# Kernel optimization log

Hardware: AMD Instinct MI355X
Metric: run time of the kernel (lower is better)

Reference implementation:

```python
import jax, jax.numpy as jnp
import numpy as np

K, B, S, D, V, H = 4, 64, 50, 256, 40000, 4
DH = D // H
TOPK = 2
NEG = -1e9
SCALE = float(1.0 / np.sqrt(DH))


def setup_inputs() -> dict:
    key = jax.random.key(0)
    ks = jax.random.split(key, 16)
    s = 0.05
    return {
        "ids":   jax.random.randint(ks[0], (K, B, S), 0, V),
        "items": jax.random.randint(ks[1], (K, B, S), 0, V),
        "adj":   jax.random.randint(ks[2], (B, S, S), 0, 5),
        "alias": jax.random.randint(ks[3], (B, S), 0, S),
        "eps":   jax.random.normal(ks[4], (B, S, K), jnp.float32),
        "emb":   jax.random.normal(ks[5], (K, V, D), jnp.float32) * s,
        "agg_a": jax.random.normal(ks[6], (K, 4, D), jnp.float32) * s,
        "Wq": jax.random.normal(ks[7], (K, D, D), jnp.float32) * s,
        "Wk": jax.random.normal(ks[8], (K, D, D), jnp.float32) * s,
        "Wv": jax.random.normal(ks[9], (K, D, D), jnp.float32) * s,
        "Wo": jax.random.normal(ks[10], (K, D, D), jnp.float32) * s,
        "ln1_g": jnp.ones((K, D), jnp.float32),
        "ln1_b": jnp.zeros((K, D), jnp.float32),
        "W1": jax.random.normal(ks[11], (K, D, 4 * D), jnp.float32) * s,
        "W2": jax.random.normal(ks[12], (K, 4 * D, D), jnp.float32) * s,
        "ln2_g": jnp.ones((K, D), jnp.float32),
        "ln2_b": jnp.zeros((K, D), jnp.float32),
        "Wg": jax.random.normal(ks[13], (D, K), jnp.float32) * s,
        "Wn": jax.random.normal(ks[14], (D, K), jnp.float32) * s,
    }


def _layer_norm(x, g, b):
    m = jnp.mean(x, -1, keepdims=True)
    v = jnp.var(x, -1, keepdims=True)
    return (x - m) * jax.lax.rsqrt(v + 1e-5) * g + b


def _per_key(ids, items, emb, a, Wq, Wk, Wv, Wo, g1, b1, W1, W2, g2, b2, adj, alias):
    hg = emb[items]                                          # [B,S,D] graph-node embeddings
    # LocalAggregator: relation-typed pairwise attention over session graph (adj in {1..4})
    e = jnp.einsum('bid,bjd,rd->rbij', hg, hg, a)            # [4,B,S,S], avoids [B,S,S,D]
    e = jax.nn.leaky_relu(e, 0.2)
    alpha = jnp.full(adj.shape, NEG, e.dtype)
    for r in range(4):
        alpha = jnp.where(adj == r + 1, e[r], alpha)
    alpha = jax.nn.softmax(alpha, -1)
    h_local = jnp.einsum('bij,bjd->bid', alpha, hg)          # graph aggregation
    h = jnp.take_along_axis(h_local, alias[..., None], axis=1)   # distribute graph rows to sequence
    # memory-transformer block (pre-LN causal MHA + FFN)
    x = _layer_norm(h, g1, b1)
    q = (x @ Wq).reshape(B, S, H, DH)
    k = (x @ Wk).reshape(B, S, H, DH)
    v = (x @ Wv).reshape(B, S, H, DH)
    scores = jnp.einsum('bihd,bjhd->bhij', q, k) * SCALE
    causal = jnp.tril(jnp.ones((S, S), bool))
    scores = jnp.where(causal, scores, NEG)
    attn = jax.nn.softmax(scores, -1)
    o = jnp.einsum('bhij,bjhd->bihd', attn, v).reshape(B, S, D) @ Wo
    h = h + o
    y = _layer_norm(h, g2, b2)
    h = h + jax.nn.gelu(y @ W1) @ W2
    return h


def reference(ids, items, adj, alias, eps, emb, agg_a, Wq, Wk, Wv, Wo,
              ln1_g, ln1_b, W1, W2, ln2_g, ln2_b, Wg, Wn):
    per_key = jax.vmap(_per_key, in_axes=(0,) * 14 + (None, None))
    h_keys = per_key(ids, items, emb, agg_a, Wq, Wk, Wv, Wo,
                     ln1_g, ln1_b, W1, W2, ln2_g, ln2_b, adj, alias)   # [K,B,S,D]
    # gate input: mean over per-key input-sequence embeddings (h_seq in original)
    h_seq = jax.vmap(lambda e, i: e[i])(emb, ids).mean(0)              # [B,S,D]
    # noisy top-k gating over node-type experts
    logits = h_seq @ Wg + jax.nn.softplus(h_seq @ Wn) * eps            # [B,S,K]
    top_v, top_i = jax.lax.top_k(logits, TOPK)
    w = jax.nn.softmax(top_v, -1)                                      # [B,S,TOPK]
    gates = jnp.sum(jax.nn.one_hot(top_i, K, dtype=w.dtype) * w[..., None], axis=-2)  # [B,S,K]
    return jnp.einsum('bsk,kbsd->bsd', gates, h_keys)
```

## Files before the change

kernel.cpp:

```cpp
#include <hip/hip_runtime.h>
#include <hip/hip_bf16.h>
#include <math.h>

#define K_ 4
#define B_ 64
#define S_ 50
#define D_ 256
#define V_ 40000
#define H_ 4
#define DH_ 64
#define NEG_ (-1e9f)
#define SCALE_ 0.125f

typedef __attribute__((ext_vector_type(8))) __bf16 bf16x8v;
typedef __attribute__((ext_vector_type(4))) float f32x4v;

__device__ __forceinline__ float wred_sum(float v) {
#pragma unroll
  for (int off = 32; off > 0; off >>= 1) v += __shfl_xor(v, off, 64);
  return v;
}
__device__ __forceinline__ float wred_max(float v) {
#pragma unroll
  for (int off = 32; off > 0; off >>= 1) v = fmaxf(v, __shfl_xor(v, off, 64));
  return v;
}
__device__ __forceinline__ float softplusf(float x) {
  return (x > 20.f) ? x : log1pf(expf(x));
}
__device__ __forceinline__ float geluf(float x) {
  const float c = 0.7978845608028654f;
  float x3 = x * x * x;
  return 0.5f * x * (1.f + tanhf(c * (x + 0.044715f * x3)));
}
__device__ __forceinline__ float bf2f(unsigned int u) {
  return __uint_as_float(u << 16);
}
__device__ __forceinline__ unsigned short f2bf(float f) {
  unsigned u = __float_as_uint(f);
  return (unsigned short)((u + 0x7fffu + ((u >> 16) & 1u)) >> 16);
}
__device__ __forceinline__ bf16x8v cvt8(float4 a, float4 b) {
  bf16x8v r;
  r[0] = (__bf16)a.x; r[1] = (__bf16)a.y; r[2] = (__bf16)a.z; r[3] = (__bf16)a.w;
  r[4] = (__bf16)b.x; r[5] = (__bf16)b.y; r[6] = (__bf16)b.z; r[7] = (__bf16)b.w;
  return r;
}

__global__ __launch_bounds__(256) void front_kernel(
    const int* __restrict__ items, const int* __restrict__ adj,
    const float* __restrict__ emb, const float* __restrict__ agg_a,
    const int* __restrict__ alias_, float* __restrict__ hbuf,
    unsigned short* __restrict__ xb,
    const float* __restrict__ ln1g, const float* __restrict__ ln1b,
    const int* __restrict__ ids, const float* __restrict__ Wg,
    const float* __restrict__ Wn, const float* __restrict__ eps,
    float* __restrict__ gates,
    const float* __restrict__ wq, const float* __restrict__ wk,
    const float* __restrict__ wv, const float* __restrict__ wo,
    const float* __restrict__ w1, const float* __restrict__ w2,
    unsigned short* __restrict__ wqkvT, unsigned short* __restrict__ woT,
    unsigned short* __restrict__ w1T, unsigned short* __restrict__ w2T) {
  __shared__ __align__(16) char smem[62816];
  int bid = blockIdx.x;
  int t = threadIdx.x;

  if (bid < 256) {
    typedef __bf16 (*arr264)[264];
    arr264 hgb = (arr264)smem;
    float (*e_f)[68] = (float(*)[68])(smem + 33792);
    unsigned char (*adj_s)[64] = (unsigned char(*)[64])(smem + 47392);
    arr264 a_sb = (arr264)(smem + 51488);
    __bf16 (*alp)[72] = (__bf16(*)[72])(smem + 53600);
    float* hl = (float*)smem;

    int kb = bid;
    int k = kb >> 6, b = kb & 63;
    for (int c = t; c < 2048; c += 256) {
      int row = c >> 5, c8 = (c & 31) * 8;
      bf16x8v val;
      if (row < S_) {
        int g = items[kb * S_ + row];
        const float* src = emb + ((long)k * V_ + g) * D_ + c8;
        val = cvt8(*(const float4*)src, *(const float4*)(src + 4));
      } else {
#pragma unroll
        for (int e = 0; e < 8; ++e) val[e] = (__bf16)0.f;
      }
      *(bf16x8v*)&hgb[row][c8] = val;
    }
    if (t < 128) {
      int row = t >> 5, c8 = (t & 31) * 8;
      const float* src = agg_a + ((long)k * 4 + row) * D_ + c8;
      *(bf16x8v*)&a_sb[row][c8] = cvt8(*(const float4*)src, *(const float4*)(src + 4));
    }
    for (int c = t; c < 4096; c += 256) {
      int i = c >> 6, j = c & 63;
      adj_s[i][j] = (i < S_ && j < S_)
                        ? (unsigned char)adj[((long)b * S_ + i) * S_ + j] : 0;
    }
    __syncthreads();
    int w = t >> 6, lane = t & 63;
    int m16 = lane & 15, quad = lane >> 4;
    float e_sel[4][4];
#pragma unroll
    for (int nt = 0; nt < 4; ++nt)
#pragma unroll
      for (int rg = 0; rg < 4; ++rg) e_sel[nt][rg] = NEG_;
#pragma unroll
    for (int r = 0; r < 4; ++r) {
      f32x4v acc[4];
#pragma unroll
      for (int nt = 0; nt < 4; ++nt) acc[nt] = (f32x4v){0.f, 0.f, 0.f, 0.f};
#pragma unroll
      for (int k0 = 0; k0 < 8; ++k0) {
        int kc = k0 * 32 + quad * 8;
        bf16x8v hr = *(const bf16x8v*)&hgb[w * 16 + m16][kc];
        bf16x8v ar = *(const bf16x8v*)&a_sb[r][kc];
        bf16x8v af;
#pragma unroll
        for (int e = 0; e < 8; ++e) af[e] = (__bf16)((float)hr[e] * (float)ar[e]);
#pragma unroll
        for (int nt = 0; nt < 4; ++nt) {
          bf16x8v bf = *(const bf16x8v*)&hgb[nt * 16 + m16][kc];
          acc[nt] = __builtin_amdgcn_mfma_f32_16x16x32_bf16(af, bf, acc[nt], 0, 0, 0);
        }
      }
#pragma unroll
      for (int nt = 0; nt < 4; ++nt)
#pragma unroll
        for (int rg = 0; rg < 4; ++rg) {
          int i = w * 16 + quad * 4 + rg, j = nt * 16 + m16;
          if (adj_s[i][j] == r + 1) {
            float v = acc[nt][rg];
            e_sel[nt][rg] = (v >= 0.f) ? v : 0.2f * v;
          }
        }
    }
#pragma unroll
    for (int nt = 0; nt < 4; ++nt)
#pragma unroll
      for (int rg = 0; rg < 4; ++rg) {
        int i = w * 16 + quad * 4 + rg;
        if (i < S_) e_f[i][nt * 16 + m16] = e_sel[nt][rg];
      }
    __syncthreads();
    for (int i = w; i < S_; i += 4) {
      float val = (lane < S_) ? e_f[i][lane] : -INFINITY;
      float m = wred_max(val);
      float p = expf(val - m);
      float ssum = wred_sum(p);
      alp[i][lane] = (__bf16)(p / ssum);
    }
    __syncthreads();
    f32x4v acc16[16];
#pragma unroll
    for (int nt = 0; nt < 16; ++nt) {
      f32x4v acc = (f32x4v){0.f, 0.f, 0.f, 0.f};
#pragma unroll
      for (int k0 = 0; k0 < 2; ++k0) {
        int jb = k0 * 32 + quad * 8;
        bf16x8v af = *(const bf16x8v*)&alp[w * 16 + m16][jb];
        bf16x8v bf;
#pragma unroll
        for (int tt = 0; tt < 8; ++tt) bf[tt] = hgb[jb + tt][nt * 16 + m16];
        acc = __builtin_amdgcn_mfma_f32_16x16x32_bf16(af, bf, acc, 0, 0, 0);
      }
      acc16[nt] = acc;
    }
    __syncthreads();
#pragma unroll
    for (int nt = 0; nt < 16; ++nt)
#pragma unroll
      for (int rg = 0; rg < 4; ++rg) {
        int i = w * 16 + quad * 4 + rg;
        if (i < S_) hl[i * 260 + nt * 16 + m16] = acc16[nt][rg];
      }
    __syncthreads();
    for (int s = w; s < S_; s += 4) {
      int src = alias_[b * S_ + s];
      const float4 v = *(const float4*)&hl[src * 260 + lane * 4];
      long off = ((long)kb * S_ + s) * D_ + lane * 4;
      *(float4*)(hbuf + off) = v;
      float sum = wred_sum(v.x + v.y + v.z + v.w);
      float sq = wred_sum(v.x * v.x + v.y * v.y + v.z * v.z + v.w * v.w);
      float mean = sum * (1.f / D_);
      float var = sq * (1.f / D_) - mean * mean;
      float rs = rsqrtf(var + 1e-5f);
      const float4 gv = *(const float4*)(ln1g + k * D_ + lane * 4);
      const float4 bv = *(const float4*)(ln1b + k * D_ + lane * 4);
      ushort4 o;
      o.x = f2bf((v.x - mean) * rs * gv.x + bv.x);
      o.y = f2bf((v.y - mean) * rs * gv.y + bv.y);
      o.z = f2bf((v.z - mean) * rs * gv.z + bv.z);
      o.w = f2bf((v.w - mean) * rs * gv.w + bv.w);
      *(ushort4*)(xb + off) = o;
    }
    return;
  }

  if (bid < 1024) {
    int tid = bid - 256;
    typedef unsigned short row66[66];
    row66* tile = (row66*)smem;
    const float* src; unsigned short* dst; int C, R; int r0, c0;
    if (tid < 192) {
      int sect = tid >> 6; int rem = tid & 63;
      int k = rem >> 4, t2 = rem & 15;
      r0 = (t2 >> 2) * 64; c0 = (t2 & 3) * 64;
      src = ((sect == 0) ? wq : (sect == 1) ? wk : wv) + (long)k * 65536;
      dst = wqkvT + ((long)k * 768 + sect * 256) * 256;
      R = 256; C = 256;
    } else if (tid < 256) {
      int rem = tid - 192; int k = rem >> 4, t2 = rem & 15;
      r0 = (t2 >> 2) * 64; c0 = (t2 & 3) * 64;
      src = wo + (long)k * 65536; dst = woT + (long)k * 65536;
      R = 256; C = 256;
    } else if (tid < 512) {
      int rem = tid - 256; int k = rem >> 6, t2 = rem & 63;
      r0 = (t2 >> 4) * 64; c0 = (t2 & 15) * 64;
      src = w1 + (long)k * 262144; dst = w1T + (long)k * 262144;
      R = 256; C = 1024;
    } else {
      int rem = tid - 512; int k = rem >> 6, t2 = rem & 63;
      r0 = (t2 >> 2) * 64; c0 = (t2 & 3) * 64;
      src = w2 + (long)k * 262144; dst = w2T + (long)k * 262144;
      R = 1024; C = 256;
    }
    int sr = t >> 2, sc = (t & 3) * 16;
    const float* p = src + (long)(r0 + sr) * C + c0 + sc;
#pragma unroll
    for (int q = 0; q < 4; ++q) {
      float4 f = *(const float4*)(p + q * 4);
      tile[sr][sc + q * 4 + 0] = f2bf(f.x);
      tile[sr][sc + q * 4 + 1] = f2bf(f.y);
      tile[sr][sc + q * 4 + 2] = f2bf(f.z);
      tile[sr][sc + q * 4 + 3] = f2bf(f.w);
    }
    __syncthreads();
    int dc = t >> 2, ch = (t & 3) * 16;
    unsigned int wds[8];
#pragma unroll
    for (int i = 0; i < 8; ++i)
      wds[i] = (unsigned int)tile[ch + 2 * i][dc] |
               ((unsigned int)tile[ch + 2 * i + 1][dc] << 16);
    unsigned short* dp = dst + (long)(c0 + dc) * R + r0 + ch;
    uint4 o0 = make_uint4(wds[0], wds[1], wds[2], wds[3]);
    uint4 o1 = make_uint4(wds[4], wds[5], wds[6], wds[7]);
    *(uint4*)dp = o0;
    *(uint4*)(dp + 8) = o1;
    return;
  }

  {
    int w = t >> 6, lane = t & 63;
    int item = (bid - 1024) * 4 + w;
    int b = item / S_, s = item % S_;
    int d0 = lane * 4;
    float4 hs = make_float4(0.f, 0.f, 0.f, 0.f);
#pragma unroll
    for (int k = 0; k < K_; ++k) {
      int id = ids[(k * B_ + b) * S_ + s];
      const float4 e = *(const float4*)(emb + ((long)k * V_ + id) * D_ + d0);
      hs.x += e.x; hs.y += e.y; hs.z += e.z; hs.w += e.w;
    }
    hs.x *= 0.25f; hs.y *= 0.25f; hs.z *= 0.25f; hs.w *= 0.25f;
    float logit[4];
#pragma unroll
    for (int j = 0; j < K_; ++j) {
      float pg = hs.x * Wg[(d0 + 0) * K_ + j] + hs.y * Wg[(d0 + 1) * K_ + j] +
                 hs.z * Wg[(d0 + 2) * K_ + j] + hs.w * Wg[(d0 + 3) * K_ + j];
      float pn = hs.x * Wn[(d0 + 0) * K_ + j] + hs.y * Wn[(d0 + 1) * K_ + j] +
                 hs.z * Wn[(d0 + 2) * K_ + j] + hs.w * Wn[(d0 + 3) * K_ + j];
      pg = wred_sum(pg);
      pn = wred_sum(pn);
      logit[j] = pg + softplusf(pn) * eps[item * K_ + j];
    }
    if (lane == 0) {
      int i0 = 0; float v0 = logit[0];
      for (int j = 1; j < K_; ++j) if (logit[j] > v0) { v0 = logit[j]; i0 = j; }
      int i1 = -1; float v1 = 0.f;
      for (int j = 0; j < K_; ++j)
        if (j != i0 && (i1 < 0 || logit[j] > v1)) { v1 = logit[j]; i1 = j; }
      float w0 = 1.f / (1.f + expf(v1 - v0));
      float w1 = 1.f - w0;
#pragma unroll
      for (int j = 0; j < K_; ++j)
        gates[item * K_ + j] = (j == i0) ? w0 : ((j == i1) ? w1 : 0.f);
    }
  }
}

__global__ __launch_bounds__(256) void bgemm3(
    const unsigned short* __restrict__ A, const unsigned short* __restrict__ Bt,
    long strideA, long strideBt, int N, int Kd,
    unsigned short* __restrict__ Cb, long strideCb, int act) {
  __shared__ unsigned short sA[128][72];
  __shared__ unsigned short sB[128][72];
  int z = blockIdx.z;
  A += (long)z * strideA;
  Bt += (long)z * strideBt;
  int t = threadIdx.x, w = t >> 6, lane = t & 63;
  int wr = w >> 1, wc = w & 1;
  int row0 = blockIdx.y * 128, col0 = blockIdx.x * 128;
  int m16 = lane & 15, quad = lane >> 4;
  f32x4v acc[4][4];
#pragma unroll
  for (int mr = 0; mr < 4; ++mr)
#pragma unroll
    for (int nr = 0; nr < 4; ++nr) acc[mr][nr] = (f32x4v){0.f, 0.f, 0.f, 0.f};
  int sr = t >> 1, sc = (t & 1) * 32;
  const unsigned short* pa = A + (long)(row0 + sr) * Kd + sc;
  const unsigned short* pb = Bt + (long)(col0 + sr) * Kd + sc;
  uint4 a0 = *(const uint4*)(pa);
  uint4 a1 = *(const uint4*)(pa + 8);
  uint4 a2 = *(const uint4*)(pa + 16);
  uint4 a3 = *(const uint4*)(pa + 24);
  uint4 b0 = *(const uint4*)(pb);
  uint4 b1 = *(const uint4*)(pb + 8);
  uint4 b2 = *(const uint4*)(pb + 16);
  uint4 b3 = *(const uint4*)(pb + 24);
  for (int k0 = 0; k0 < Kd; k0 += 64) {
    __syncthreads();
    *(uint4*)&sA[sr][sc] = a0;
    *(uint4*)&sA[sr][sc + 8] = a1;
    *(uint4*)&sA[sr][sc + 16] = a2;
    *(uint4*)&sA[sr][sc + 24] = a3;
    *(uint4*)&sB[sr][sc] = b0;
    *(uint4*)&sB[sr][sc + 8] = b1;
    *(uint4*)&sB[sr][sc + 16] = b2;
    *(uint4*)&sB[sr][sc + 24] = b3;
    if (k0 + 64 < Kd) {
      a0 = *(const uint4*)(pa + k0 + 64);
      a1 = *(const uint4*)(pa + k0 + 72);
      a2 = *(const uint4*)(pa + k0 + 80);
      a3 = *(const uint4*)(pa + k0 + 88);
      b0 = *(const uint4*)(pb + k0 + 64);
      b1 = *(const uint4*)(pb + k0 + 72);
      b2 = *(const uint4*)(pb + k0 + 80);
      b3 = *(const uint4*)(pb + k0 + 88);
    }
    __syncthreads();
#pragma unroll
    for (int half = 0; half < 2; ++half) {
      int kg = half * 32 + quad * 8;
      bf16x8v af[4], bf[4];
#pragma unroll
      for (int i = 0; i < 4; ++i) {
        af[i] = *(const bf16x8v*)&sA[wr * 64 + i * 16 + m16][kg];
        bf[i] = *(const bf16x8v*)&sB[wc * 64 + i * 16 + m16][kg];
      }
#pragma unroll
      for (int mr = 0; mr < 4; ++mr)
#pragma unroll
        for (int nr = 0; nr < 4; ++nr)
          acc[mr][nr] = __builtin_amdgcn_mfma_f32_16x16x32_bf16(
              af[mr], bf[nr], acc[mr][nr], 0, 0, 0);
    }
  }
#pragma unroll
  for (int mr = 0; mr < 4; ++mr) {
    int rbase = row0 + wr * 64 + mr * 16 + quad * 4;
#pragma unroll
    for (int nr = 0; nr < 4; ++nr) {
      int col = col0 + wc * 64 + nr * 16 + m16;
#pragma unroll
      for (int i2 = 0; i2 < 4; ++i2) {
        float vv = acc[mr][nr][i2];
        if (act == 1) vv = geluf(vv);
        Cb[(long)z * strideCb + (long)(rbase + i2) * N + col] = f2bf(vv);
      }
    }
  }
}

__global__ __launch_bounds__(256) void attn_mfma(
    const unsigned short* __restrict__ qkv, unsigned short* __restrict__ o) {
  __shared__ __bf16 qs[64][72], ks[64][72], vs[64][72];
  __shared__ __bf16 psh[64][72], psl[64][72];
  int idx = blockIdx.x;
  int h = idx & 3;
  int kb = idx >> 2;
  long base = (long)kb * S_ * 768 + h * DH_;
  int t = threadIdx.x;
  for (int f = t; f < 512; f += 256) {
    int row = f >> 3, c8 = (f & 7) * 8;
    uint4 zq = make_uint4(0, 0, 0, 0), zk = zq, zv = zq;
    if (row < S_) {
      long g = base + (long)row * 768 + c8;
      zq = *(const uint4*)(qkv + g);
      zk = *(const uint4*)(qkv + g + 256);
      zv = *(const uint4*)(qkv + g + 512);
    }
    *(uint4*)&qs[row][c8] = zq;
    *(uint4*)&ks[row][c8] = zk;
    *(uint4*)&vs[row][c8] = zv;
  }
  __syncthreads();
  int w = t >> 6, lane = t & 63;
  int m16 = lane & 15, quad = lane >> 4;
  f32x4v sacc[4];
#pragma unroll
  for (int nt = 0; nt < 4; ++nt) sacc[nt] = (f32x4v){0.f, 0.f, 0.f, 0.f};
#pragma unroll
  for (int k0 = 0; k0 < 2; ++k0) {
    int kc = k0 * 32 + quad * 8;
    bf16x8v af = *(const bf16x8v*)&qs[w * 16 + m16][kc];
#pragma unroll
    for (int nt = 0; nt < 4; ++nt) {
      bf16x8v bf = *(const bf16x8v*)&ks[nt * 16 + m16][kc];
      sacc[nt] = __builtin_amdgcn_mfma_f32_16x16x32_bf16(af, bf, sacc[nt], 0, 0, 0);
    }
  }
#pragma unroll
  for (int rg = 0; rg < 4; ++rg) {
    int i = w * 16 + quad * 4 + rg;
    float v4[4];
    if (i < S_) {
      float mx = -INFINITY;
#pragma unroll
      for (int nt = 0; nt < 4; ++nt) {
        int j = nt * 16 + m16;
        float vv = (j <= i) ? sacc[nt][rg] * SCALE_ : -INFINITY;
        v4[nt] = vv;
        mx = fmaxf(mx, vv);
      }
#pragma unroll
      for (int off = 1; off < 16; off <<= 1)
        mx = fmaxf(mx, __shfl_xor(mx, off, 64));
      float sum = 0.f;
#pragma unroll
      for (int nt = 0; nt < 4; ++nt) {
        v4[nt] = expf(v4[nt] - mx);
        sum += v4[nt];
      }
#pragma unroll
      for (int off = 1; off < 16; off <<= 1) sum += __shfl_xor(sum, off, 64);
      float inv = 1.f / sum;
#pragma unroll
      for (int nt = 0; nt < 4; ++nt) v4[nt] *= inv;
    } else {
#pragma unroll
      for (int nt = 0; nt < 4; ++nt) v4[nt] = 0.f;
    }
#pragma unroll
    for (int nt = 0; nt < 4; ++nt) {
      __bf16 hi = (__bf16)v4[nt];
      psh[i][nt * 16 + m16] = hi;
      psl[i][nt * 16 + m16] = (__bf16)(v4[nt] - (float)hi);
    }
  }
  __syncthreads();
  f32x4v oacc[4];
#pragma unroll
  for (int nt = 0; nt < 4; ++nt) oacc[nt] = (f32x4v){0.f, 0.f, 0.f, 0.f};
#pragma unroll
  for (int k0 = 0; k0 < 2; ++k0) {
    int jb = k0 * 32 + quad * 8;
    bf16x8v ah = *(const bf16x8v*)&psh[w * 16 + m16][jb];
    bf16x8v al = *(const bf16x8v*)&psl[w * 16 + m16][jb];
#pragma unroll
    for (int nt = 0; nt < 4; ++nt) {
      bf16x8v bf;
#pragma unroll
      for (int tt = 0; tt < 8; ++tt) bf[tt] = vs[jb + tt][nt * 16 + m16];
      oacc[nt] = __builtin_amdgcn_mfma_f32_16x16x32_bf16(ah, bf, oacc[nt], 0, 0, 0);
      oacc[nt] = __builtin_amdgcn_mfma_f32_16x16x32_bf16(al, bf, oacc[nt], 0, 0, 0);
    }
  }
#pragma unroll
  for (int nt = 0; nt < 4; ++nt)
#pragma unroll
    for (int rg = 0; rg < 4; ++rg) {
      int i = w * 16 + quad * 4 + rg;
      if (i < S_)
        o[((long)kb * S_ + i) * D_ + h * DH_ + nt * 16 + m16] = f2bf(oacc[nt][rg]);
    }
}

__global__ __launch_bounds__(256) void bgemm_oln(
    const unsigned short* __restrict__ A, const unsigned short* __restrict__ Bt,
    float* __restrict__ hbuf, unsigned short* __restrict__ y,
    const float* __restrict__ g2, const float* __restrict__ b2) {
  __shared__ unsigned short sA[64][72];
  __shared__ unsigned short sB[256][72];
  const long BSD = (long)B_ * S_ * D_;
  int z = blockIdx.z;
  const unsigned short* Ap = A + (long)z * BSD;
  const unsigned short* Bp = Bt + (long)z * 65536;
  int t = threadIdx.x, w = t >> 6, lane = t & 63;
  int row0 = blockIdx.x * 64;
  int m16 = lane & 15, quad = lane >> 4;
  f32x4v acc[16];
#pragma unroll
  for (int nt = 0; nt < 16; ++nt) acc[nt] = (f32x4v){0.f, 0.f, 0.f, 0.f};
  int sr = t >> 2, sc = (t & 3) * 16;
  const unsigned short* pa = Ap + (long)(row0 + sr) * 256 + sc;
  const unsigned short* pb = Bp + (long)sr * 256 + sc;
  uint4 a0 = *(const uint4*)pa;
  uint4 a1 = *(const uint4*)(pa + 8);
  uint4 bv[8];
#pragma unroll
  for (int q = 0; q < 4; ++q) {
    bv[2 * q] = *(const uint4*)(pb + q * 16384);
    bv[2 * q + 1] = *(const uint4*)(pb + q * 16384 + 8);
  }
  for (int k0 = 0; k0 < 256; k0 += 64) {
    __syncthreads();
    *(uint4*)&sA[sr][sc] = a0;
    *(uint4*)&sA[sr][sc + 8] = a1;
#pragma unroll
    for (int q = 0; q < 4; ++q) {
      *(uint4*)&sB[q * 64 + sr][sc] = bv[2 * q];
      *(uint4*)&sB[q * 64 + sr][sc + 8] = bv[2 * q + 1];
    }
    if (k0 + 64 < 256) {
      a0 = *(const uint4*)(pa + k0 + 64);
      a1 = *(const uint4*)(pa + k0 + 72);
#pragma unroll
      for (int q = 0; q < 4; ++q) {
        bv[2 * q] = *(const uint4*)(pb + q * 16384 + k0 + 64);
        bv[2 * q + 1] = *(const uint4*)(pb + q * 16384 + k0 + 72);
      }
    }
    __syncthreads();
#pragma unroll
    for (int half = 0; half < 2; ++half) {
      int kg = half * 32 + quad * 8;
      bf16x8v af = *(const bf16x8v*)&sA[w * 16 + m16][kg];
#pragma unroll
      for (int nt = 0; nt < 16; ++nt) {
        bf16x8v bf = *(const bf16x8v*)&sB[nt * 16 + m16][kg];
        acc[nt] = __builtin_amdgcn_mfma_f32_16x16x32_bf16(af, bf, acc[nt], 0, 0, 0);
      }
    }
  }
  long zoff = (long)z * BSD;
  int rbase = row0 + w * 16 + quad * 4;
#pragma unroll
  for (int nt = 0; nt < 16; ++nt)
#pragma unroll
    for (int i2 = 0; i2 < 4; ++i2) {
      long off = zoff + (long)(rbase + i2) * 256 + nt * 16 + m16;
      float vv = acc[nt][i2] + hbuf[off];
      acc[nt][i2] = vv;
      hbuf[off] = vv;
    }
  float mean[4], rstd[4];
#pragma unroll
  for (int i2 = 0; i2 < 4; ++i2) {
    float s = 0.f, q = 0.f;
#pragma unroll
    for (int nt = 0; nt < 16; ++nt) {
      float vv = acc[nt][i2];
      s += vv; q += vv * vv;
    }
#pragma unroll
    for (int off = 1; off < 16; off <<= 1) {
      s += __shfl_xor(s, off, 64);
      q += __shfl_xor(q, off, 64);
    }
    float m = s * (1.f / D_);
    float var = q * (1.f / D_) - m * m;
    mean[i2] = m;
    rstd[i2] = rsqrtf(var + 1e-5f);
  }
#pragma unroll
  for (int nt = 0; nt < 16; ++nt) {
    float gv = g2[z * D_ + nt * 16 + m16];
    float bvv = b2[z * D_ + nt * 16 + m16];
#pragma unroll
    for (int i2 = 0; i2 < 4; ++i2) {
      long off = zoff + (long)(rbase + i2) * 256 + nt * 16 + m16;
      y[off] = f2bf((acc[nt][i2] - mean[i2]) * rstd[i2] * gv + bvv);
    }
  }
}

__global__ __launch_bounds__(256) void bgemm_f2a(
    const unsigned short* __restrict__ A, const unsigned short* __restrict__ Bt,
    const float* __restrict__ hbuf, const float* __restrict__ gates,
    float* __restrict__ out) {
  __shared__ unsigned short sA[64][72];
  __shared__ unsigned short sB[64][72];
  const long T4 = 3276800;
  const long BSD = (long)B_ * S_ * D_;
  int z = blockIdx.z;
  int t = threadIdx.x, w = t >> 6, lane = t & 63;
  int col0 = blockIdx.x * 64, row0 = blockIdx.y * 64;
  int m16 = lane & 15, quad = lane >> 4;
  f32x4v acc[4];
#pragma unroll
  for (int nt = 0; nt < 4; ++nt) acc[nt] = (f32x4v){0.f, 0.f, 0.f, 0.f};
  int sr = t >> 2, sc = (t & 3) * 16;
  const unsigned short* pa = A + (long)z * T4 + (long)(row0 + sr) * 1024 + sc;
  const unsigned short* pb = Bt + (long)z * 262144 + (long)(col0 + sr) * 1024 + sc;
  uint4 a0 = *(const uint4*)pa;
  uint4 a1 = *(const uint4*)(pa + 8);
  uint4 b0 = *(const uint4*)pb;
  uint4 b1 = *(const uint4*)(pb + 8);
  for (int k0 = 0; k0 < 1024; k0 += 64) {
    __syncthreads();
    *(uint4*)&sA[sr][sc] = a0;
    *(uint4*)&sA[sr][sc + 8] = a1;
    *(uint4*)&sB[sr][sc] = b0;
    *(uint4*)&sB[sr][sc + 8] = b1;
    if (k0 + 64 < 1024) {
      a0 = *(const uint4*)(pa + k0 + 64);
      a1 = *(const uint4*)(pa + k0 + 72);
      b0 = *(const uint4*)(pb + k0 + 64);
      b1 = *(const uint4*)(pb + k0 + 72);
    }
    __syncthreads();
#pragma unroll
    for (int half = 0; half < 2; ++half) {
      int kg = half * 32 + quad * 8;
      bf16x8v af = *(const bf16x8v*)&sA[w * 16 + m16][kg];
#pragma unroll
      for (int nt = 0; nt < 4; ++nt) {
        bf16x8v bf = *(const bf16x8v*)&sB[nt * 16 + m16][kg];
        acc[nt] = __builtin_amdgcn_mfma_f32_16x16x32_bf16(af, bf, acc[nt], 0, 0, 0);
      }
    }
  }
  int rbase = row0 + w * 16 + quad * 4;
#pragma unroll
  for (int i2 = 0; i2 < 4; ++i2) {
    float gz = gates[(rbase + i2) * 4 + z];
    if (gz != 0.f) {
#pragma unroll
      for (int nt = 0; nt < 4; ++nt) {
        long off = (long)(rbase + i2) * 256 + col0 + nt * 16 + m16;
        float vv = gz * (acc[nt][i2] + hbuf[(long)z * BSD + off]);
        atomicAdd(&out[off], vv);
      }
    }
  }
}

extern "C" void kernel_launch(void* const* d_in, const int* in_sizes, int n_in,
                              void* d_out, int out_size, void* d_ws,
                              size_t ws_size, hipStream_t stream) {
  const int* ids = (const int*)d_in[0];
  const int* items = (const int*)d_in[1];
  const int* adj = (const int*)d_in[2];
  const int* alias = (const int*)d_in[3];
  const float* eps = (const float*)d_in[4];
  const float* emb = (const float*)d_in[5];
  const float* agg_a = (const float*)d_in[6];
  const float* Wq = (const float*)d_in[7];
  const float* Wk = (const float*)d_in[8];
  const float* Wv = (const float*)d_in[9];
  const float* Wo = (const float*)d_in[10];
  const float* ln1g = (const float*)d_in[11];
  const float* ln1b = (const float*)d_in[12];
  const float* W1 = (const float*)d_in[13];
  const float* W2 = (const float*)d_in[14];
  const float* ln2g = (const float*)d_in[15];
  const float* ln2b = (const float*)d_in[16];
  const float* Wg = (const float*)d_in[17];
  const float* Wn = (const float*)d_in[18];
  float* out = (float*)d_out;

  const long BSD = (long)B_ * S_ * D_;
  float* ws = (float*)d_ws;
  float* gates = ws;
  float* hbuf = ws + 16384;
  unsigned short* ub = (unsigned short*)(ws + 16384 + 4 * BSD);
  unsigned short* xb = ub;
  unsigned short* qkvb = ub + 3276800;
  unsigned short* tb = qkvb;
  unsigned short* wqkvT = ub + 16384000;
  unsigned short* woT = wqkvT + 786432;
  unsigned short* w1T = woT + 262144;
  unsigned short* w2T = w1T + 1048576;

  const long T4 = 3276800;

  hipMemsetAsync(out, 0, (size_t)BSD * sizeof(float), stream);

  front_kernel<<<1824, 256, 0, stream>>>(
      items, adj, emb, agg_a, alias, hbuf, xb, ln1g, ln1b,
      ids, Wg, Wn, eps, gates,
      Wq, Wk, Wv, Wo, W1, W2, wqkvT, woT, w1T, w2T);
  bgemm3<<<dim3(6, 25, 4), 256, 0, stream>>>(xb, wqkvT, BSD, 196608, 768, 256,
      qkvb, 2457600, 0);
  attn_mfma<<<K_ * B_ * H_, 256, 0, stream>>>(qkvb, xb);
  bgemm_oln<<<dim3(50, 1, 4), 256, 0, stream>>>(xb, woT, hbuf, xb, ln2g, ln2b);
  bgemm3<<<dim3(8, 25, 4), 256, 0, stream>>>(xb, w1T, BSD, 262144, 1024, 256,
      tb, T4, 1);
  bgemm_f2a<<<dim3(4, 50, 4), 256, 0, stream>>>(tb, w2T, hbuf, gates, out);
}
```

Baseline: 398.0 us.

## Fuse QKV projection into attention and fuse the whole post-attention tail per (key,batch)

The QKV GEMM is folded into the attention kernel: each (key,batch,head) block computes its Q, K and V tiles straight into LDS from bf16 activations and weights read from global memory. The output projection, residual add, LayerNorm, FFN1 with GELU, FFN2 and the gated atomic accumulation are merged into a single kernel with one block per (key,batch), so the hidden activation stays in LDS. This removes three launches and the global round trips for qkv, o, y and the 1024-wide FFN intermediate. In exchange the tail runs only 256 blocks with weights streamed from global/L2 without LDS staging, which risks low occupancy and latency-bound GEMMs. Activation reads for rows 50 to 63 of each tile run past the valid sequence rows.

```diff
diff --git a/kernel.cpp b/kernel.cpp
--- a/kernel.cpp
+++ b/kernel.cpp
@@ -32,9 +32,6 @@
   const float c = 0.7978845608028654f;
   float x3 = x * x * x;
   return 0.5f * x * (1.f + tanhf(c * (x + 0.044715f * x3)));
-}
-__device__ __forceinline__ float bf2f(unsigned int u) {
-  return __uint_as_float(u << 16);
 }
 __device__ __forceinline__ unsigned short f2bf(float f) {
   unsigned u = __float_as_uint(f);
@@ -291,114 +288,45 @@
   }
 }
 
-__global__ __launch_bounds__(256) void bgemm3(
-    const unsigned short* __restrict__ A, const unsigned short* __restrict__ Bt,
-    long strideA, long strideBt, int N, int Kd,
-    unsigned short* __restrict__ Cb, long strideCb, int act) {
-  __shared__ unsigned short sA[128][72];
-  __shared__ unsigned short sB[128][72];
-  int z = blockIdx.z;
-  A += (long)z * strideA;
-  Bt += (long)z * strideBt;
-  int t = threadIdx.x, w = t >> 6, lane = t & 63;
-  int wr = w >> 1, wc = w & 1;
-  int row0 = blockIdx.y * 128, col0 = blockIdx.x * 128;
-  int m16 = lane & 15, quad = lane >> 4;
-  f32x4v acc[4][4];
-#pragma unroll
-  for (int mr = 0; mr < 4; ++mr)
-#pragma unroll
-    for (int nr = 0; nr < 4; ++nr) acc[mr][nr] = (f32x4v){0.f, 0.f, 0.f, 0.f};
-  int sr = t >> 1, sc = (t & 1) * 32;
-  const unsigned short* pa = A + (long)(row0 + sr) * Kd + sc;
-  const unsigned short* pb = Bt + (long)(col0 + sr) * Kd + sc;
-  uint4 a0 = *(const uint4*)(pa);
-  uint4 a1 = *(const uint4*)(pa + 8);
-  uint4 a2 = *(const uint4*)(pa + 16);
-  uint4 a3 = *(const uint4*)(pa + 24);
-  uint4 b0 = *(const uint4*)(pb);
-  uint4 b1 = *(const uint4*)(pb + 8);
-  uint4 b2 = *(const uint4*)(pb + 16);
-  uint4 b3 = *(const uint4*)(pb + 24);
-  for (int k0 = 0; k0 < Kd; k0 += 64) {
-    __syncthreads();
-    *(uint4*)&sA[sr][sc] = a0;
-    *(uint4*)&sA[sr][sc + 8] = a1;
-    *(uint4*)&sA[sr][sc + 16] = a2;
-    *(uint4*)&sA[sr][sc + 24] = a3;
-    *(uint4*)&sB[sr][sc] = b0;
-    *(uint4*)&sB[sr][sc + 8] = b1;
-    *(uint4*)&sB[sr][sc + 16] = b2;
-    *(uint4*)&sB[sr][sc + 24] = b3;
-    if (k0 + 64 < Kd) {
-      a0 = *(const uint4*)(pa + k0 + 64);
-      a1 = *(const uint4*)(pa + k0 + 72);
-      a2 = *(const uint4*)(pa + k0 + 80);
-      a3 = *(const uint4*)(pa + k0 + 88);
-      b0 = *(const uint4*)(pb + k0 + 64);
-      b1 = *(const uint4*)(pb + k0 + 72);
-      b2 = *(const uint4*)(pb + k0 + 80);
-      b3 = *(const uint4*)(pb + k0 + 88);
-    }
-    __syncthreads();
-#pragma unroll
-    for (int half = 0; half < 2; ++half) {
-      int kg = half * 32 + quad * 8;
-      bf16x8v af[4], bf[4];
-#pragma unroll
-      for (int i = 0; i < 4; ++i) {
-        af[i] = *(const bf16x8v*)&sA[wr * 64 + i * 16 + m16][kg];
-        bf[i] = *(const bf16x8v*)&sB[wc * 64 + i * 16 + m16][kg];
-      }
-#pragma unroll
-      for (int mr = 0; mr < 4; ++mr)
-#pragma unroll
-        for (int nr = 0; nr < 4; ++nr)
-          acc[mr][nr] = __builtin_amdgcn_mfma_f32_16x16x32_bf16(
-              af[mr], bf[nr], acc[mr][nr], 0, 0, 0);
-    }
-  }
-#pragma unroll
-  for (int mr = 0; mr < 4; ++mr) {
-    int rbase = row0 + wr * 64 + mr * 16 + quad * 4;
-#pragma unroll
-    for (int nr = 0; nr < 4; ++nr) {
-      int col = col0 + wc * 64 + nr * 16 + m16;
-#pragma unroll
-      for (int i2 = 0; i2 < 4; ++i2) {
-        float vv = acc[mr][nr][i2];
-        if (act == 1) vv = geluf(vv);
-        Cb[(long)z * strideCb + (long)(rbase + i2) * N + col] = f2bf(vv);
-      }
-    }
-  }
-}
-
-__global__ __launch_bounds__(256) void attn_mfma(
-    const unsigned short* __restrict__ qkv, unsigned short* __restrict__ o) {
+__global__ __launch_bounds__(256) void qkv_attn(
+    const unsigned short* __restrict__ xb,
+    const unsigned short* __restrict__ wqkvT,
+    unsigned short* __restrict__ ob) {
   __shared__ __bf16 qs[64][72], ks[64][72], vs[64][72];
   __shared__ __bf16 psh[64][72], psl[64][72];
   int idx = blockIdx.x;
-  int h = idx & 3;
-  int kb = idx >> 2;
-  long base = (long)kb * S_ * 768 + h * DH_;
-  int t = threadIdx.x;
-  for (int f = t; f < 512; f += 256) {
-    int row = f >> 3, c8 = (f & 7) * 8;
-    uint4 zq = make_uint4(0, 0, 0, 0), zk = zq, zv = zq;
-    if (row < S_) {
-      long g = base + (long)row * 768 + c8;
-      zq = *(const uint4*)(qkv + g);
-      zk = *(const uint4*)(qkv + g + 256);
-      zv = *(const uint4*)(qkv + g + 512);
-    }
-    *(uint4*)&qs[row][c8] = zq;
-    *(uint4*)&ks[row][c8] = zk;
-    *(uint4*)&vs[row][c8] = zv;
+  int h = idx & 3, kb = idx >> 2;
+  int k = kb >> 6;
+  int t = threadIdx.x, w = t >> 6, lane = t & 63;
+  int m16 = lane & 15, quad = lane >> 4;
+  const unsigned short* xrow = xb + (long)kb * S_ * D_;
+#pragma unroll
+  for (int sect = 0; sect < 3; ++sect) {
+    f32x4v acc[4];
+#pragma unroll
+    for (int mr = 0; mr < 4; ++mr) acc[mr] = (f32x4v){0.f, 0.f, 0.f, 0.f};
+    const unsigned short* wrow =
+        wqkvT + ((long)k * 768 + sect * 256 + h * 64 + w * 16 + m16) * 256;
+#pragma unroll
+    for (int st = 0; st < 8; ++st) {
+      int kc = st * 32 + quad * 8;
+      bf16x8v bf = *(const bf16x8v*)(wrow + kc);
+#pragma unroll
+      for (int mr = 0; mr < 4; ++mr) {
+        bf16x8v af = *(const bf16x8v*)(xrow + (long)(mr * 16 + m16) * 256 + kc);
+        acc[mr] = __builtin_amdgcn_mfma_f32_16x16x32_bf16(af, bf, acc[mr], 0, 0, 0);
+      }
+    }
+    __bf16 (*dst)[72] = (sect == 0) ? qs : (sect == 1) ? ks : vs;
+#pragma unroll
+    for (int mr = 0; mr < 4; ++mr)
+#pragma unroll
+      for (int i2 = 0; i2 < 4; ++i2)
+        dst[mr * 16 + quad * 4 + i2][w * 16 + m16] = (__bf16)acc[mr][i2];
   }
   __syncthreads();
-  int w = t >> 6, lane = t & 63;
-  int m16 = lane & 15, quad = lane >> 4;
+  for (int c = t; c < 14 * 72; c += 256) vs[50 + c / 72][c % 72] = (__bf16)0.f;
+  __syncthreads();
   f32x4v sacc[4];
 #pragma unroll
   for (int nt = 0; nt < 4; ++nt) sacc[nt] = (f32x4v){0.f, 0.f, 0.f, 0.f};
@@ -474,168 +402,165 @@
     for (int rg = 0; rg < 4; ++rg) {
       int i = w * 16 + quad * 4 + rg;
       if (i < S_)
-        o[((long)kb * S_ + i) * D_ + h * DH_ + nt * 16 + m16] = f2bf(oacc[nt][rg]);
-    }
-}
-
-__global__ __launch_bounds__(256) void bgemm_oln(
-    const unsigned short* __restrict__ A, const unsigned short* __restrict__ Bt,
-    float* __restrict__ hbuf, unsigned short* __restrict__ y,
-    const float* __restrict__ g2, const float* __restrict__ b2) {
-  __shared__ unsigned short sA[64][72];
-  __shared__ unsigned short sB[256][72];
-  const long BSD = (long)B_ * S_ * D_;
-  int z = blockIdx.z;
-  const unsigned short* Ap = A + (long)z * BSD;
-  const unsigned short* Bp = Bt + (long)z * 65536;
+        ob[((long)kb * S_ + i) * D_ + h * DH_ + nt * 16 + m16] = f2bf(oacc[nt][rg]);
+    }
+}
+
+__global__ __launch_bounds__(256) void tail_fused(
+    const unsigned short* __restrict__ ob, const unsigned short* __restrict__ woT,
+    const unsigned short* __restrict__ w1T, const unsigned short* __restrict__ w2T,
+    const float* __restrict__ hbuf, const float* __restrict__ gates,
+    const float* __restrict__ g2, const float* __restrict__ b2,
+    float* __restrict__ out) {
+  __shared__ __bf16 ybuf[64][264];
+  __shared__ __bf16 ts[64][136];
+  __shared__ float lnS[4][64], lnQ[4][64];
+  int kb = blockIdx.x;
+  int k = kb >> 6, b = kb & 63;
   int t = threadIdx.x, w = t >> 6, lane = t & 63;
-  int row0 = blockIdx.x * 64;
   int m16 = lane & 15, quad = lane >> 4;
-  f32x4v acc[16];
-#pragma unroll
-  for (int nt = 0; nt < 16; ++nt) acc[nt] = (f32x4v){0.f, 0.f, 0.f, 0.f};
-  int sr = t >> 2, sc = (t & 3) * 16;
-  const unsigned short* pa = Ap + (long)(row0 + sr) * 256 + sc;
-  const unsigned short* pb = Bp + (long)sr * 256 + sc;
-  uint4 a0 = *(const uint4*)pa;
-  uint4 a1 = *(const uint4*)(pa + 8);
-  uint4 bv[8];
-#pragma unroll
-  for (int q = 0; q < 4; ++q) {
-    bv[2 * q] = *(const uint4*)(pb + q * 16384);
-    bv[2 * q + 1] = *(const uint4*)(pb + q * 16384 + 8);
-  }
-  for (int k0 = 0; k0 < 256; k0 += 64) {
-    __syncthreads();
-    *(uint4*)&sA[sr][sc] = a0;
-    *(uint4*)&sA[sr][sc + 8] = a1;
-#pragma unroll
-    for (int q = 0; q < 4; ++q) {
-      *(uint4*)&sB[q * 64 + sr][sc] = bv[2 * q];
-      *(uint4*)&sB[q * 64 + sr][sc + 8] = bv[2 * q + 1];
-    }
-    if (k0 + 64 < 256) {
-      a0 = *(const uint4*)(pa + k0 + 64);
-      a1 = *(const uint4*)(pa + k0 + 72);
-#pragma unroll
-      for (int q = 0; q < 4; ++q) {
-        bv[2 * q] = *(const uint4*)(pb + q * 16384 + k0 + 64);
-        bv[2 * q + 1] = *(const uint4*)(pb + q * 16384 + k0 + 72);
-      }
-    }
-    __syncthreads();
-#pragma unroll
-    for (int half = 0; half < 2; ++half) {
-      int kg = half * 32 + quad * 8;
-      bf16x8v af = *(const bf16x8v*)&sA[w * 16 + m16][kg];
-#pragma unroll
-      for (int nt = 0; nt < 16; ++nt) {
-        bf16x8v bf = *(const bf16x8v*)&sB[nt * 16 + m16][kg];
-        acc[nt] = __builtin_amdgcn_mfma_f32_16x16x32_bf16(af, bf, acc[nt], 0, 0, 0);
-      }
-    }
-  }
-  long zoff = (long)z * BSD;
-  int rbase = row0 + w * 16 + quad * 4;
-#pragma unroll
-  for (int nt = 0; nt < 16; ++nt)
+  for (int c = t; c < 14 * 264; c += 256) ybuf[50 + c / 264][c % 264] = (__bf16)0.f;
+  f32x4v v[4][4];
+#pragma unroll
+  for (int mr = 0; mr < 4; ++mr)
+#pragma unroll
+    for (int nt = 0; nt < 4; ++nt) v[mr][nt] = (f32x4v){0.f, 0.f, 0.f, 0.f};
+  const unsigned short* orow = ob + (long)kb * S_ * D_;
+#pragma unroll
+  for (int st = 0; st < 8; ++st) {
+    int kc = st * 32 + quad * 8;
+    bf16x8v bfv[4];
+#pragma unroll
+    for (int nt = 0; nt < 4; ++nt)
+      bfv[nt] = *(const bf16x8v*)(woT + ((long)k * 256 + w * 64 + nt * 16 + m16) * 256 + kc);
+#pragma unroll
+    for (int mr = 0; mr < 4; ++mr) {
+      bf16x8v af = *(const bf16x8v*)(orow + (long)(mr * 16 + m16) * 256 + kc);
+#pragma unroll
+      for (int nt = 0; nt < 4; ++nt)
+        v[mr][nt] = __builtin_amdgcn_mfma_f32_16x16x32_bf16(af, bfv[nt], v[mr][nt], 0, 0, 0);
+    }
+  }
+  long hb = (long)kb * S_ * D_;
+#pragma unroll
+  for (int mr = 0; mr < 4; ++mr)
 #pragma unroll
     for (int i2 = 0; i2 < 4; ++i2) {
-      long off = zoff + (long)(rbase + i2) * 256 + nt * 16 + m16;
-      float vv = acc[nt][i2] + hbuf[off];
-      acc[nt][i2] = vv;
-      hbuf[off] = vv;
-    }
-  float mean[4], rstd[4];
-#pragma unroll
-  for (int i2 = 0; i2 < 4; ++i2) {
-    float s = 0.f, q = 0.f;
-#pragma unroll
-    for (int nt = 0; nt < 16; ++nt) {
-      float vv = acc[nt][i2];
-      s += vv; q += vv * vv;
-    }
-#pragma unroll
-    for (int off = 1; off < 16; off <<= 1) {
-      s += __shfl_xor(s, off, 64);
-      q += __shfl_xor(q, off, 64);
-    }
-    float m = s * (1.f / D_);
-    float var = q * (1.f / D_) - m * m;
-    mean[i2] = m;
-    rstd[i2] = rsqrtf(var + 1e-5f);
-  }
-#pragma unroll
-  for (int nt = 0; nt < 16; ++nt) {
-    float gv = g2[z * D_ + nt * 16 + m16];
-    float bvv = b2[z * D_ + nt * 16 + m16];
+      int row = mr * 16 + quad * 4 + i2;
+      float s = 0.f, q = 0.f;
+#pragma unroll
+      for (int nt = 0; nt < 4; ++nt) {
+        int col = w * 64 + nt * 16 + m16;
+        float hv = (row < S_) ? hbuf[hb + (long)row * 256 + col] : 0.f;
+        float vv = v[mr][nt][i2] + hv;
+        v[mr][nt][i2] = vv;
+        s += vv; q += vv * vv;
+      }
+#pragma unroll
+      for (int off = 1; off < 16; off <<= 1) {
+        s += __shfl_xor(s, off, 64);
+        q += __shfl_xor(q, off, 64);
+      }
+      if (m16 == 0) { lnS[w][row] = s; lnQ[w][row] = q; }
+    }
+  __syncthreads();
+  float gv[4], bvv[4];
+#pragma unroll
+  for (int nt = 0; nt < 4; ++nt) {
+    int col = w * 64 + nt * 16 + m16;
+    gv[nt] = g2[k * D_ + col];
+    bvv[nt] = b2[k * D_ + col];
+  }
+#pragma unroll
+  for (int mr = 0; mr < 4; ++mr)
 #pragma unroll
     for (int i2 = 0; i2 < 4; ++i2) {
-      long off = zoff + (long)(rbase + i2) * 256 + nt * 16 + m16;
-      y[off] = f2bf((acc[nt][i2] - mean[i2]) * rstd[i2] * gv + bvv);
-    }
-  }
-}
-
-__global__ __launch_bounds__(256) void bgemm_f2a(
-    const unsigned short* __restrict__ A, const unsigned short* __restrict__ Bt,
-    const float* __restrict__ hbuf, const float* __restrict__ gates,
-    float* __restrict__ out) {
-  __shared__ unsigned short sA[64][72];
-  __shared__ unsigned short sB[64][72];
-  const long T4 = 3276800;
-  const long BSD = (long)B_ * S_ * D_;
-  int z = blockIdx.z;
-  int t = threadIdx.x, w = t >> 6, lane = t & 63;
-  int col0 = blockIdx.x * 64, row0 = blockIdx.y * 64;
-  int m16 = lane & 15, quad = lane >> 4;
-  f32x4v acc[4];
-#pragma unroll
-  for (int nt = 0; nt < 4; ++nt) acc[nt] = (f32x4v){0.f, 0.f, 0.f, 0.f};
-  int sr = t >> 2, sc = (t & 3) * 16;
-  const unsigned short* pa = A + (long)z * T4 + (long)(row0 + sr) * 1024 + sc;
-  const unsigned short* pb = Bt + (long)z * 262144 + (long)(col0 + sr) * 1024 + sc;
-  uint4 a0 = *(const uint4*)pa;
-  uint4 a1 = *(const uint4*)(pa + 8);
-  uint4 b0 = *(const uint4*)pb;
-  uint4 b1 = *(const uint4*)(pb + 8);
-  for (int k0 = 0; k0 < 1024; k0 += 64) {
-    __syncthreads();
-    *(uint4*)&sA[sr][sc] = a0;
-    *(uint4*)&sA[sr][sc + 8] = a1;
-    *(uint4*)&sB[sr][sc] = b0;
-    *(uint4*)&sB[sr][sc + 8] = b1;
-    if (k0 + 64 < 1024) {
-      a0 = *(const uint4*)(pa + k0 + 64);
-      a1 = *(const uint4*)(pa + k0 + 72);
-      b0 = *(const uint4*)(pb + k0 + 64);
-      b1 = *(const uint4*)(pb + k0 + 72);
-    }
-    __syncthreads();
-#pragma unroll
-    for (int half = 0; half < 2; ++half) {
-      int kg = half * 32 + quad * 8;
-      bf16x8v af = *(const bf16x8v*)&sA[w * 16 + m16][kg];
+      int row = mr * 16 + quad * 4 + i2;
+      if (row < S_) {
+        float s = lnS[0][row] + lnS[1][row] + lnS[2][row] + lnS[3][row];
+        float q = lnQ[0][row] + lnQ[1][row] + lnQ[2][row] + lnQ[3][row];
+        float mean = s * (1.f / D_);
+        float var = q * (1.f / D_) - mean * mean;
+        float rs = rsqrtf(var + 1e-5f);
+#pragma unroll
+        for (int nt = 0; nt < 4; ++nt)
+          ybuf[row][w * 64 + nt * 16 + m16] =
+              (__bf16)((v[mr][nt][i2] - mean) * rs * gv[nt] + bvv[nt]);
+      }
+    }
+  __syncthreads();
+  f32x4v racc[4][4];
+#pragma unroll
+  for (int mr = 0; mr < 4; ++mr)
+#pragma unroll
+    for (int nt = 0; nt < 4; ++nt) racc[mr][nt] = (f32x4v){0.f, 0.f, 0.f, 0.f};
+  for (int c = 0; c < 8; ++c) {
+    f32x4v a1[4][2];
+#pragma unroll
+    for (int mr = 0; mr < 4; ++mr)
+#pragma unroll
+      for (int ct = 0; ct < 2; ++ct) a1[mr][ct] = (f32x4v){0.f, 0.f, 0.f, 0.f};
+#pragma unroll
+    for (int st = 0; st < 8; ++st) {
+      int kc = st * 32 + quad * 8;
+      bf16x8v bf1[2];
+#pragma unroll
+      for (int ct = 0; ct < 2; ++ct) {
+        int n = c * 128 + w * 32 + ct * 16 + m16;
+        bf1[ct] = *(const bf16x8v*)(w1T + ((long)k * 1024 + n) * 256 + kc);
+      }
+#pragma unroll
+      for (int mr = 0; mr < 4; ++mr) {
+        bf16x8v af = *(const bf16x8v*)&ybuf[mr * 16 + m16][kc];
+#pragma unroll
+        for (int ct = 0; ct < 2; ++ct)
+          a1[mr][ct] = __builtin_amdgcn_mfma_f32_16x16x32_bf16(af, bf1[ct], a1[mr][ct], 0, 0, 0);
+      }
+    }
+    __syncthreads();
+#pragma unroll
+    for (int mr = 0; mr < 4; ++mr)
+#pragma unroll
+      for (int ct = 0; ct < 2; ++ct)
+#pragma unroll
+        for (int i2 = 0; i2 < 4; ++i2)
+          ts[mr * 16 + quad * 4 + i2][w * 32 + ct * 16 + m16] =
+              (__bf16)geluf(a1[mr][ct][i2]);
+    __syncthreads();
+#pragma unroll
+    for (int ks = 0; ks < 4; ++ks) {
+      int kc = ks * 32 + quad * 8;
+      bf16x8v bf2[4];
 #pragma unroll
       for (int nt = 0; nt < 4; ++nt) {
-        bf16x8v bf = *(const bf16x8v*)&sB[nt * 16 + m16][kg];
-        acc[nt] = __builtin_amdgcn_mfma_f32_16x16x32_bf16(af, bf, acc[nt], 0, 0, 0);
-      }
-    }
-  }
-  int rbase = row0 + w * 16 + quad * 4;
-#pragma unroll
-  for (int i2 = 0; i2 < 4; ++i2) {
-    float gz = gates[(rbase + i2) * 4 + z];
-    if (gz != 0.f) {
-#pragma unroll
-      for (int nt = 0; nt < 4; ++nt) {
-        long off = (long)(rbase + i2) * 256 + col0 + nt * 16 + m16;
-        float vv = gz * (acc[nt][i2] + hbuf[(long)z * BSD + off]);
-        atomicAdd(&out[off], vv);
-      }
-    }
-  }
+        int n = w * 64 + nt * 16 + m16;
+        bf2[nt] = *(const bf16x8v*)(w2T + ((long)k * 256 + n) * 1024 + c * 128 + kc);
+      }
+#pragma unroll
+      for (int mr = 0; mr < 4; ++mr) {
+        bf16x8v af = *(const bf16x8v*)&ts[mr * 16 + m16][kc];
+#pragma unroll
+        for (int nt = 0; nt < 4; ++nt)
+          racc[mr][nt] = __builtin_amdgcn_mfma_f32_16x16x32_bf16(af, bf2[nt], racc[mr][nt], 0, 0, 0);
+      }
+    }
+  }
+#pragma unroll
+  for (int mr = 0; mr < 4; ++mr)
+#pragma unroll
+    for (int i2 = 0; i2 < 4; ++i2) {
+      int row = mr * 16 + quad * 4 + i2;
+      if (row < S_) {
+        float gz = gates[(b * S_ + row) * 4 + k];
+        if (gz != 0.f) {
+#pragma unroll
+          for (int nt = 0; nt < 4; ++nt) {
+            long off = (long)(b * S_ + row) * 256 + w * 64 + nt * 16 + m16;
+            atomicAdd(&out[off], gz * (racc[mr][nt][i2] + v[mr][nt][i2]));
+          }
+        }
+      }
+    }
 }
 
 extern "C" void kernel_launch(void* const* d_in, const int* in_sizes, int n_in,
@@ -668,26 +593,19 @@
   float* hbuf = ws + 16384;
   unsigned short* ub = (unsigned short*)(ws + 16384 + 4 * BSD);
   unsigned short* xb = ub;
-  unsigned short* qkvb = ub + 3276800;
-  unsigned short* tb = qkvb;
+  unsigned short* obuf = ub + 3276800;
   unsigned short* wqkvT = ub + 16384000;
   unsigned short* woT = wqkvT + 786432;
   unsigned short* w1T = woT + 262144;
   unsigned short* w2T = w1T + 1048576;
 
-  const long T4 = 3276800;
-
   hipMemsetAsync(out, 0, (size_t)BSD * sizeof(float), stream);
 
   front_kernel<<<1824, 256, 0, stream>>>(
       items, adj, emb, agg_a, alias, hbuf, xb, ln1g, ln1b,
       ids, Wg, Wn, eps, gates,
       Wq, Wk, Wv, Wo, W1, W2, wqkvT, woT, w1T, w2T);
-  bgemm3<<<dim3(6, 25, 4), 256, 0, stream>>>(xb, wqkvT, BSD, 196608, 768, 256,
-      qkvb, 2457600, 0);
-  attn_mfma<<<K_ * B_ * H_, 256, 0, stream>>>(qkvb, xb);
-  bgemm_oln<<<dim3(50, 1, 4), 256, 0, stream>>>(xb, woT, hbuf, xb, ln2g, ln2b);
-  bgemm3<<<dim3(8, 25, 4), 256, 0, stream>>>(xb, w1T, BSD, 262144, 1024, 256,
-      tb, T4, 1);
-  bgemm_f2a<<<dim3(4, 50, 4), 256, 0, stream>>>(tb, w2T, hbuf, gates, out);
-}
+  qkv_attn<<<K_ * B_ * H_, 256, 0, stream>>>(xb, wqkvT, obuf);
+  tail_fused<<<K_ * B_, 256, 0, stream>>>(obuf, woT, w1T, w2T, hbuf, gates,
+                                          ln2g, ln2b, out);
+}
```

After: 443.9 us. 1.12x slower.
